# Performance work log

Hardware: AMD Instinct MI355X
Metric: run time of the kernel (lower is better)

## Reference

```python
import jax, jax.numpy as jnp
import numpy as np

NUM_ROUNDS = 3


def squash(x, axis=-1):
    # s_norm / (1 + s_norm) * x / sqrt(s_norm), matching the torch code exactly
    s_norm = jnp.sum(x * x, axis=axis, keepdims=True)
    return (s_norm / (1.0 + s_norm)) * x / jnp.sqrt(s_norm)


def setup_inputs() -> dict:
    key = jax.random.key(0)
    k1, k2 = jax.random.split(key)
    x = jax.random.normal(k1, (512, 1152, 8), dtype=jnp.float32)   # [B, R, Cin]
    W = jax.random.normal(k2, (10, 1152, 8, 16), dtype=jnp.float32)  # [N, R, Cin, Cout]
    return {"x": x, "W": W}


def reference(x, W):
    # priors = x[None,:,:,None,:] @ W[:,None,:,:,:]  -> [N, B, R, 1, Cout]
    priors = jnp.einsum('bri,nrio->nbro', x, W)[:, :, :, None, :]
    logits = jnp.zeros_like(priors)  # [N, B, R, 1, Cout]
    outps = None
    for i in range(NUM_ROUNDS):
        probs = jax.nn.softmax(logits, axis=2)  # softmax over routes R
        outps = squash(jnp.sum(probs * priors, axis=2, keepdims=True))  # [N, B, 1, 1, Cout]
        if i != NUM_ROUNDS - 1:
            # agreement logit update: dot over Cout
            logits = logits + jnp.sum(priors * outps, axis=-1, keepdims=True)
    return outps
```

## Files before the change

kernel.cpp:

```cpp
#include <hip/hip_runtime.h>
#include <math.h>

#define R_ROUTES 1152
#define CIN 8
#define COUT 16
#define BATCH 512
#define NCAPS 10
#define NUM_ROUNDS 3

typedef __fp16 h2 __attribute__((ext_vector_type(2)));
union U32H2 { unsigned int u; h2 h; };

__device__ __forceinline__ unsigned int pkrtz(float lo, float hi) {
    U32H2 v; v.h = __builtin_amdgcn_cvt_pkrtz(lo, hi);
    return v.u;
}
__device__ __forceinline__ h2 as_h2(unsigned int u) { U32H2 v; v.u = u; return v.h; }
__device__ __forceinline__ float f_lo(unsigned int u) { return (float)as_h2(u).x; }
__device__ __forceinline__ float f_hi(unsigned int u) { return (float)as_h2(u).y; }
__device__ __forceinline__ float dot2(unsigned int p, unsigned int s, float c) {
    return __builtin_amdgcn_fdot2(as_h2(p), as_h2(s), c, false);
}

#define DPP_XOR1 0xB1
#define DPP_XOR2 0x4E
#define DPP_ROR4 0x124
#define DPP_ROR8 0x128
template<int CTRL>
__device__ __forceinline__ float dpp_add(float v) {
    int d = __builtin_amdgcn_update_dpp(0, __float_as_int(v), CTRL, 0xf, 0xf, false);
    return v + __int_as_float(d);
}
__device__ __forceinline__ float p16_add(float v) {
    float a = v, b = v;
    asm("v_permlane16_swap_b32 %0, %1" : "+v"(a), "+v"(b));
    return a + b;
}
__device__ __forceinline__ float p32_add(float v) {
    float a = v, b = v;
    asm("v_permlane32_swap_b32 %0, %1" : "+v"(a), "+v"(b));
    return a + b;
}
__device__ __forceinline__ float wave_sum64(float v) {
    v = dpp_add<DPP_XOR1>(v);
    v = dpp_add<DPP_XOR2>(v);
    v = dpp_add<DPP_ROR4>(v);
    v = dpp_add<DPP_ROR8>(v);
    v = p16_add(v);
    return p32_add(v);
}

__device__ __forceinline__ int sunit(int r, int h) {
    return (2 * r + h) ^ ((r >> 2) & 7);
}

extern "C" __global__ void __launch_bounds__(256)
pack_wx(const float* __restrict__ W, const float* __restrict__ x,
        unsigned int* __restrict__ Wp, uint4* __restrict__ Xp)
{
    const int blk = blockIdx.x;
    if (blk < 720) {
        const int tau = blk * 256 + threadIdx.x;
        const int o = tau & 15;
        const int nr = tau >> 4;
        const float* __restrict__ src = W + (size_t)nr * 128 + o;
        uint4 u;
        u.x = pkrtz(src[0],  src[16]);
        u.y = pkrtz(src[32], src[48]);
        u.z = pkrtz(src[64], src[80]);
        u.w = pkrtz(src[96], src[112]);
        *(uint4*)(Wp + (size_t)tau * 4) = u;
    } else {
        const int idx = (blk - 720) * 256 + threadIdx.x;
        const float4 a = *(const float4*)(x + (size_t)idx * 8);
        const float4 b = *(const float4*)(x + (size_t)idx * 8 + 4);
        uint4 u;
        u.x = pkrtz(a.x, a.y);
        u.y = pkrtz(a.z, a.w);
        u.z = pkrtz(b.x, b.y);
        u.w = pkrtz(b.z, b.w);
        Xp[idx] = u;
    }
}

template<bool XP>
__global__ void __launch_bounds__(512, 4)
capsule_routing_v15(const float* __restrict__ x,
                    const unsigned int* __restrict__ Wp,
                    const uint4* __restrict__ Xp,
                    float* __restrict__ out)
{
    __shared__ __align__(16) unsigned int pbuf[2 * R_ROUTES * 8];
    __shared__ __align__(16) float wred[16 * 16];
    __shared__ __align__(16) float red[2 * 32 * 20];
    __shared__ float sred[2 * 4];
    __shared__ __align__(16) float sv[2 * 16];

    const int blk = blockIdx.x;
    const int n = blk >> 8;
    const int bp = blk & 255;
    const int t = threadIdx.x;

    const unsigned int* __restrict__ Wn = Wp + (size_t)n * (R_ROUTES * 64);

    float cs[2][4] = {{0.f, 0.f, 0.f, 0.f}, {0.f, 0.f, 0.f, 0.f}};
    {
        const int q = t >> 2;
        const int oq = t & 3;
        const int subw = (oq & 1) * 2;
        const int hq = oq >> 1;

        const float* __restrict__ x0 = x + (size_t)(2 * bp) * (R_ROUTES * CIN);
        const float* __restrict__ x1 = x0 + R_ROUTES * CIN;
        const uint4* __restrict__ xq0 = Xp + (size_t)(2 * bp) * R_ROUTES;
        const uint4* __restrict__ xq1 = xq0 + R_ROUTES;

        uint4 wA0, wA1, wA2, wA3, wB0, wB1, wB2, wB3;
        uint4 xA0, xA1, xB0, xB1;
        float4 gA0, gA1, gA2, gA3, gB0, gB1, gB2, gB3;

        auto loadW = [&](int it, uint4& a0, uint4& a1, uint4& a2, uint4& a3) {
            const unsigned int* wb = Wn + (size_t)(it * 128 + q) * 64 + oq * 4;
            a0 = *(const uint4*)(wb + 0);
            a1 = *(const uint4*)(wb + 16);
            a2 = *(const uint4*)(wb + 32);
            a3 = *(const uint4*)(wb + 48);
        };
        auto loadX = [&](int it, uint4& a, uint4& b,
                         float4& g0, float4& g1, float4& g2, float4& g3) {
            const int r = it * 128 + q;
            if constexpr (XP) {
                a = xq0[r];
                b = xq1[r];
            } else {
                g0 = *(const float4*)(x0 + r * 8);
                g1 = *(const float4*)(x0 + r * 8 + 4);
                g2 = *(const float4*)(x1 + r * 8);
                g3 = *(const float4*)(x1 + r * 8 + 4);
            }
        };
        auto packX = [&](uint4& a, uint4& b,
                         float4 g0, float4 g1, float4 g2, float4 g3) {
            if constexpr (!XP) {
                a.x = pkrtz(g0.x, g0.y); a.y = pkrtz(g0.z, g0.w);
                a.z = pkrtz(g1.x, g1.y); a.w = pkrtz(g1.z, g1.w);
                b.x = pkrtz(g2.x, g2.y); b.y = pkrtz(g2.z, g2.w);
                b.z = pkrtz(g3.x, g3.y); b.w = pkrtz(g3.z, g3.w);
            }
        };
        auto compute = [&](int it, uint4 w0, uint4 w1, uint4 w2, uint4 w3,
                           uint4 xa, uint4 xb) {
            const int r = it * 128 + q;
            {
                const float p0 = dot2(w0.w, xa.w, dot2(w0.z, xa.z, dot2(w0.y, xa.y, dot2(w0.x, xa.x, 0.f))));
                const float p1 = dot2(w1.w, xa.w, dot2(w1.z, xa.z, dot2(w1.y, xa.y, dot2(w1.x, xa.x, 0.f))));
                const float p2 = dot2(w2.w, xa.w, dot2(w2.z, xa.z, dot2(w2.y, xa.y, dot2(w2.x, xa.x, 0.f))));
                const float p3 = dot2(w3.w, xa.w, dot2(w3.z, xa.z, dot2(w3.y, xa.y, dot2(w3.x, xa.x, 0.f))));
                cs[0][0] += p0; cs[0][1] += p1; cs[0][2] += p2; cs[0][3] += p3;
                uint2 u; u.x = pkrtz(p0, p1); u.y = pkrtz(p2, p3);
                *(uint2*)(pbuf + sunit(r, hq) * 4 + subw) = u;
            }
            {
                const float p0 = dot2(w0.w, xb.w, dot2(w0.z, xb.z, dot2(w0.y, xb.y, dot2(w0.x, xb.x, 0.f))));
                const float p1 = dot2(w1.w, xb.w, dot2(w1.z, xb.z, dot2(w1.y, xb.y, dot2(w1.x, xb.x, 0.f))));
                const float p2 = dot2(w2.w, xb.w, dot2(w2.z, xb.z, dot2(w2.y, xb.y, dot2(w2.x, xb.x, 0.f))));
                const float p3 = dot2(w3.w, xb.w, dot2(w3.z, xb.z, dot2(w3.y, xb.y, dot2(w3.x, xb.x, 0.f))));
                cs[1][0] += p0; cs[1][1] += p1; cs[1][2] += p2; cs[1][3] += p3;
                uint2 u; u.x = pkrtz(p0, p1); u.y = pkrtz(p2, p3);
                *(uint2*)(pbuf + R_ROUTES * 8 + sunit(r, hq) * 4 + subw) = u;
            }
        };

        loadW(0, wA0, wA1, wA2, wA3);
        loadX(0, xA0, xA1, gA0, gA1, gA2, gA3);
        #pragma unroll 1
        for (int it = 0; it < 8; it += 2) {
            loadW(it + 1, wB0, wB1, wB2, wB3);
            loadX(it + 1, xB0, xB1, gB0, gB1, gB2, gB3);
            packX(xA0, xA1, gA0, gA1, gA2, gA3);
            compute(it, wA0, wA1, wA2, wA3, xA0, xA1);
            loadW(it + 2, wA0, wA1, wA2, wA3);
            loadX(it + 2, xA0, xA1, gA0, gA1, gA2, gA3);
            packX(xB0, xB1, gB0, gB1, gB2, gB3);
            compute(it + 1, wB0, wB1, wB2, wB3, xB0, xB1);
        }
        packX(xA0, xA1, gA0, gA1, gA2, gA3);
        compute(8, wA0, wA1, wA2, wA3, xA0, xA1);

        #pragma unroll
        for (int b = 0; b < 2; ++b)
            #pragma unroll
            for (int j = 0; j < 4; ++j) {
                float v = cs[b][j];
                v = dpp_add<DPP_ROR4>(v);
                v = dpp_add<DPP_ROR8>(v);
                v = p16_add(v);
                v = p32_add(v);
                cs[b][j] = v;
            }
        if ((t & 63) < 4) {
            const int w = t >> 6;
            *(float4*)(wred + (w * 2 + 0) * 16 + 4 * oq) =
                make_float4(cs[0][0], cs[0][1], cs[0][2], cs[0][3]);
            *(float4*)(wred + (w * 2 + 1) * 16 + 4 * oq) =
                make_float4(cs[1][0], cs[1][1], cs[1][2], cs[1][3]);
        }
    }
    __syncthreads();

    const int half = t >> 8;
    const int tt = t & 255;
    unsigned int* __restrict__ pb = pbuf + half * (R_ROUTES * 8);
    float* __restrict__ redh = red + half * (32 * 20);
    float* __restrict__ sredh = sred + half * 4;
    float* __restrict__ svh = sv + half * 16;

    if (tt < 64) {
        const int k = tt & 15, wg = tt >> 4;
        float s = wred[(wg * 2 + half) * 16 + k] + wred[((wg + 4) * 2 + half) * 16 + k];
        s = p16_add(s);
        s = p32_add(s);
        if (tt < 16) svh[tt] = s * (1.0f / (float)R_ROUTES);
    }
    __syncthreads();

    float4 s0 = *(const float4*)(svh + 0);
    float4 s1 = *(const float4*)(svh + 4);
    float4 s2 = *(const float4*)(svh + 8);
    float4 s3 = *(const float4*)(svh + 12);
    float sn = s0.x * s0.x;
    sn = fmaf(s0.y, s0.y, sn); sn = fmaf(s0.z, s0.z, sn); sn = fmaf(s0.w, s0.w, sn);
    sn = fmaf(s1.x, s1.x, sn); sn = fmaf(s1.y, s1.y, sn); sn = fmaf(s1.z, s1.z, sn);
    sn = fmaf(s1.w, s1.w, sn);
    sn = fmaf(s2.x, s2.x, sn); sn = fmaf(s2.y, s2.y, sn); sn = fmaf(s2.z, s2.z, sn);
    sn = fmaf(s2.w, s2.w, sn);
    sn = fmaf(s3.x, s3.x, sn); sn = fmaf(s3.y, s3.y, sn); sn = fmaf(s3.z, s3.z, sn);
    sn = fmaf(s3.w, s3.w, sn);
    float factor = sn / ((1.0f + sn) * sqrtf(sn));

    const int nr = (tt < 128) ? 5 : 4;
    float bl[5] = {0.f, 0.f, 0.f, 0.f, 0.f};

    #pragma unroll 1
    for (int pass = 1; pass < NUM_ROUNDS; ++pass) {
        unsigned int svp[8];
        svp[0] = pkrtz(s0.x, s0.y); svp[1] = pkrtz(s0.z, s0.w);
        svp[2] = pkrtz(s1.x, s1.y); svp[3] = pkrtz(s1.z, s1.w);
        svp[4] = pkrtz(s2.x, s2.y); svp[5] = pkrtz(s2.z, s2.w);
        svp[6] = pkrtz(s3.x, s3.y); svp[7] = pkrtz(s3.z, s3.w);
        float acc[16];
        #pragma unroll
        for (int o = 0; o < 16; ++o) acc[o] = 0.f;
        float es = 0.f;

        #pragma unroll
        for (int k = 0; k < 5; ++k) {
            if (k < nr) {
                const int r = tt + (k << 8);
                const uint4 a = *(const uint4*)(pb + sunit(r, 0) * 4);
                const uint4 c = *(const uint4*)(pb + sunit(r, 1) * 4);
                float d = 0.f;
                d = dot2(a.x, svp[0], d);
                d = dot2(a.y, svp[1], d);
                d = dot2(a.z, svp[2], d);
                d = dot2(a.w, svp[3], d);
                d = dot2(c.x, svp[4], d);
                d = dot2(c.y, svp[5], d);
                d = dot2(c.z, svp[6], d);
                d = dot2(c.w, svp[7], d);
                bl[k] = fmaf(factor, d, bl[k]);
                const float e = __expf(bl[k]);
                es += e;
                acc[0]  = fmaf(e, f_lo(a.x), acc[0]);
                acc[1]  = fmaf(e, f_hi(a.x), acc[1]);
                acc[2]  = fmaf(e, f_lo(a.y), acc[2]);
                acc[3]  = fmaf(e, f_hi(a.y), acc[3]);
                acc[4]  = fmaf(e, f_lo(a.z), acc[4]);
                acc[5]  = fmaf(e, f_hi(a.z), acc[5]);
                acc[6]  = fmaf(e, f_lo(a.w), acc[6]);
                acc[7]  = fmaf(e, f_hi(a.w), acc[7]);
                acc[8]  = fmaf(e, f_lo(c.x), acc[8]);
                acc[9]  = fmaf(e, f_hi(c.x), acc[9]);
                acc[10] = fmaf(e, f_lo(c.y), acc[10]);
                acc[11] = fmaf(e, f_hi(c.y), acc[11]);
                acc[12] = fmaf(e, f_lo(c.z), acc[12]);
                acc[13] = fmaf(e, f_hi(c.z), acc[13]);
                acc[14] = fmaf(e, f_lo(c.w), acc[14]);
                acc[15] = fmaf(e, f_hi(c.w), acc[15]);
            }
        }
        es = wave_sum64(es);
        if ((t & 63) == 0) sredh[tt >> 6] = es;

        #pragma unroll
        for (int o = 0; o < 16; ++o) {
            float v = acc[o];
            v = dpp_add<DPP_XOR1>(v);
            v = dpp_add<DPP_XOR2>(v);
            v = dpp_add<DPP_ROR4>(v);
            acc[o] = v;
        }
        if ((tt & 7) == 0) {
            float* dst = redh + (tt >> 3) * 20;
            *(float4*)(dst + 0)  = make_float4(acc[0],  acc[1],  acc[2],  acc[3]);
            *(float4*)(dst + 4)  = make_float4(acc[4],  acc[5],  acc[6],  acc[7]);
            *(float4*)(dst + 8)  = make_float4(acc[8],  acc[9],  acc[10], acc[11]);
            *(float4*)(dst + 12) = make_float4(acc[12], acc[13], acc[14], acc[15]);
        }
        __syncthreads();

        if (tt < 64) {
            const int k = tt & 15, wg = tt >> 4;
            float s = 0.f;
            #pragma unroll
            for (int i = 0; i < 8; ++i) s += redh[(wg * 8 + i) * 20 + k];
            s = p16_add(s);
            s = p32_add(s);
            if (tt < 16) {
                const float Z = sredh[0] + sredh[1] + sredh[2] + sredh[3];
                svh[tt] = s / Z;
            }
        }
        __syncthreads();

        s0 = *(const float4*)(svh + 0);
        s1 = *(const float4*)(svh + 4);
        s2 = *(const float4*)(svh + 8);
        s3 = *(const float4*)(svh + 12);
        sn = s0.x * s0.x;
        sn = fmaf(s0.y, s0.y, sn); sn = fmaf(s0.z, s0.z, sn); sn = fmaf(s0.w, s0.w, sn);
        sn = fmaf(s1.x, s1.x, sn); sn = fmaf(s1.y, s1.y, sn); sn = fmaf(s1.z, s1.z, sn);
        sn = fmaf(s1.w, s1.w, sn);
        sn = fmaf(s2.x, s2.x, sn); sn = fmaf(s2.y, s2.y, sn); sn = fmaf(s2.z, s2.z, sn);
        sn = fmaf(s2.w, s2.w, sn);
        sn = fmaf(s3.x, s3.x, sn); sn = fmaf(s3.y, s3.y, sn); sn = fmaf(s3.z, s3.z, sn);
        sn = fmaf(s3.w, s3.w, sn);
        factor = sn / ((1.0f + sn) * sqrtf(sn));
    }

    if (tt < 16) {
        const int o = (tt >> 2) + ((tt & 3) << 2);
        out[((size_t)n * BATCH + 2 * bp + half) * COUT + o] = factor * svh[tt];
    }
}

extern "C" void kernel_launch(void* const* d_in, const int* in_sizes, int n_in,
                              void* d_out, int out_size, void* d_ws, size_t ws_size,
                              hipStream_t stream) {
    const float* x = (const float*)d_in[0];
    const float* W = (const float*)d_in[1];
    float* out = (float*)d_out;

    unsigned int* Wp = (unsigned int*)d_ws;
    const size_t WPB = (size_t)NCAPS * R_ROUTES * COUT * 16;
    const size_t XPB = (size_t)BATCH * R_ROUTES * 16;
    uint4* Xp = (uint4*)((char*)d_ws + WPB);

    if (ws_size >= WPB + XPB) {
        pack_wx<<<dim3(720 + 2304), dim3(256), 0, stream>>>(W, x, Wp, Xp);
        capsule_routing_v15<true><<<dim3(NCAPS * (BATCH / 2)), dim3(512), 0, stream>>>(x, Wp, Xp, out);
    } else {
        pack_wx<<<dim3(720), dim3(256), 0, stream>>>(W, x, Wp, Xp);
        capsule_routing_v15<false><<<dim3(NCAPS * (BATCH / 2)), dim3(512), 0, stream>>>(x, Wp, Xp, out);
    }
}
```

Before: 128.3 us.

## Assign one batch element per block and split routes across both halves

After: 146.3 us. 1.14x slower.

```diff
diff --git a/kernel.cpp b/kernel.cpp
--- a/kernel.cpp
+++ b/kernel.cpp
@@ -32,13 +32,19 @@
     return v + __int_as_float(d);
 }
 __device__ __forceinline__ float p16_add(float v) {
-    float a = v, b = v;
-    asm("v_permlane16_swap_b32 %0, %1" : "+v"(a), "+v"(b));
+    float a, b;
+    asm("v_mov_b32 %0, %2\n\t"
+        "v_mov_b32 %1, %2\n\t"
+        "v_permlane16_swap_b32 %0, %1"
+        : "=&v"(a), "=&v"(b) : "v"(v));
     return a + b;
 }
 __device__ __forceinline__ float p32_add(float v) {
-    float a = v, b = v;
-    asm("v_permlane32_swap_b32 %0, %1" : "+v"(a), "+v"(b));
+    float a, b;
+    asm("v_mov_b32 %0, %2\n\t"
+        "v_mov_b32 %1, %2\n\t"
+        "v_permlane32_swap_b32 %0, %1"
+        : "=&v"(a), "=&v"(b) : "v"(v));
     return a + b;
 }
 __device__ __forceinline__ float wave_sum64(float v) {
@@ -85,149 +91,116 @@
 
 template<bool XP>
 __global__ void __launch_bounds__(512, 4)
-capsule_routing_v15(const float* __restrict__ x,
+capsule_routing_v16(const float* __restrict__ x,
                     const unsigned int* __restrict__ Wp,
                     const uint4* __restrict__ Xp,
                     float* __restrict__ out)
 {
-    __shared__ __align__(16) unsigned int pbuf[2 * R_ROUTES * 8];
-    __shared__ __align__(16) float wred[16 * 16];
+    __shared__ __align__(16) unsigned int pbuf[R_ROUTES * 8];
+    __shared__ __align__(16) float wred[8 * 16];
     __shared__ __align__(16) float red[2 * 32 * 20];
-    __shared__ float sred[2 * 4];
-    __shared__ __align__(16) float sv[2 * 16];
+    __shared__ __align__(16) float sred[2 * 4];
+    __shared__ __align__(16) float sv[16];
 
     const int blk = blockIdx.x;
-    const int n = blk >> 8;
-    const int bp = blk & 255;
+    const int n = blk >> 9;
+    const int b = blk & 511;
     const int t = threadIdx.x;
 
     const unsigned int* __restrict__ Wn = Wp + (size_t)n * (R_ROUTES * 64);
 
-    float cs[2][4] = {{0.f, 0.f, 0.f, 0.f}, {0.f, 0.f, 0.f, 0.f}};
+    float cs[4] = {0.f, 0.f, 0.f, 0.f};
     {
         const int q = t >> 2;
         const int oq = t & 3;
         const int subw = (oq & 1) * 2;
         const int hq = oq >> 1;
 
-        const float* __restrict__ x0 = x + (size_t)(2 * bp) * (R_ROUTES * CIN);
-        const float* __restrict__ x1 = x0 + R_ROUTES * CIN;
-        const uint4* __restrict__ xq0 = Xp + (size_t)(2 * bp) * R_ROUTES;
-        const uint4* __restrict__ xq1 = xq0 + R_ROUTES;
+        const float* __restrict__ x0 = x + (size_t)b * (R_ROUTES * CIN);
+        const uint4* __restrict__ xq0 = Xp + (size_t)b * R_ROUTES;
 
         uint4 wA0, wA1, wA2, wA3, wB0, wB1, wB2, wB3;
-        uint4 xA0, xA1, xB0, xB1;
-        float4 gA0, gA1, gA2, gA3, gB0, gB1, gB2, gB3;
+        uint4 xA, xB;
 
         auto loadW = [&](int it, uint4& a0, uint4& a1, uint4& a2, uint4& a3) {
-            const unsigned int* wb = Wn + (size_t)(it * 128 + q) * 64 + oq * 4;
-            a0 = *(const uint4*)(wb + 0);
-            a1 = *(const uint4*)(wb + 16);
-            a2 = *(const uint4*)(wb + 32);
-            a3 = *(const uint4*)(wb + 48);
+            const unsigned int* wb = Wn + (size_t)(it * 128 + q) * 64;
+            a0 = *(const uint4*)(wb + (oq + 0) * 4);
+            a1 = *(const uint4*)(wb + (oq + 4) * 4);
+            a2 = *(const uint4*)(wb + (oq + 8) * 4);
+            a3 = *(const uint4*)(wb + (oq + 12) * 4);
         };
-        auto loadX = [&](int it, uint4& a, uint4& b,
-                         float4& g0, float4& g1, float4& g2, float4& g3) {
+        auto loadX = [&](int it, uint4& xa) {
             const int r = it * 128 + q;
             if constexpr (XP) {
-                a = xq0[r];
-                b = xq1[r];
+                xa = xq0[r];
             } else {
-                g0 = *(const float4*)(x0 + r * 8);
-                g1 = *(const float4*)(x0 + r * 8 + 4);
-                g2 = *(const float4*)(x1 + r * 8);
-                g3 = *(const float4*)(x1 + r * 8 + 4);
+                const float4 g0 = *(const float4*)(x0 + r * 8);
+                const float4 g1 = *(const float4*)(x0 + r * 8 + 4);
+                xa.x = pkrtz(g0.x, g0.y); xa.y = pkrtz(g0.z, g0.w);
+                xa.z = pkrtz(g1.x, g1.y); xa.w = pkrtz(g1.z, g1.w);
             }
         };
-        auto packX = [&](uint4& a, uint4& b,
-                         float4 g0, float4 g1, float4 g2, float4 g3) {
-            if constexpr (!XP) {
-                a.x = pkrtz(g0.x, g0.y); a.y = pkrtz(g0.z, g0.w);
-                a.z = pkrtz(g1.x, g1.y); a.w = pkrtz(g1.z, g1.w);
-                b.x = pkrtz(g2.x, g2.y); b.y = pkrtz(g2.z, g2.w);
-                b.z = pkrtz(g3.x, g3.y); b.w = pkrtz(g3.z, g3.w);
-            }
+        auto compute = [&](int it, const uint4& w0, const uint4& w1,
+                           const uint4& w2, const uint4& w3, const uint4& xa) {
+            const int r = it * 128 + q;
+            const float p0 = dot2(w0.w, xa.w, dot2(w0.z, xa.z, dot2(w0.y, xa.y, dot2(w0.x, xa.x, 0.f))));
+            const float p1 = dot2(w1.w, xa.w, dot2(w1.z, xa.z, dot2(w1.y, xa.y, dot2(w1.x, xa.x, 0.f))));
+            const float p2 = dot2(w2.w, xa.w, dot2(w2.z, xa.z, dot2(w2.y, xa.y, dot2(w2.x, xa.x, 0.f))));
+            const float p3 = dot2(w3.w, xa.w, dot2(w3.z, xa.z, dot2(w3.y, xa.y, dot2(w3.x, xa.x, 0.f))));
+            cs[0] += p0; cs[1] += p1; cs[2] += p2; cs[3] += p3;
+            uint2 u; u.x = pkrtz(p0, p1); u.y = pkrtz(p2, p3);
+            *(uint2*)(pbuf + sunit(r, hq) * 4 + subw) = u;
         };
-        auto compute = [&](int it, uint4 w0, uint4 w1, uint4 w2, uint4 w3,
-                           uint4 xa, uint4 xb) {
-            const int r = it * 128 + q;
-            {
-                const float p0 = dot2(w0.w, xa.w, dot2(w0.z, xa.z, dot2(w0.y, xa.y, dot2(w0.x, xa.x, 0.f))));
-                const float p1 = dot2(w1.w, xa.w, dot2(w1.z, xa.z, dot2(w1.y, xa.y, dot2(w1.x, xa.x, 0.f))));
-                const float p2 = dot2(w2.w, xa.w, dot2(w2.z, xa.z, dot2(w2.y, xa.y, dot2(w2.x, xa.x, 0.f))));
-                const float p3 = dot2(w3.w, xa.w, dot2(w3.z, xa.z, dot2(w3.y, xa.y, dot2(w3.x, xa.x, 0.f))));
-                cs[0][0] += p0; cs[0][1] += p1; cs[0][2] += p2; cs[0][3] += p3;
-                uint2 u; u.x = pkrtz(p0, p1); u.y = pkrtz(p2, p3);
-                *(uint2*)(pbuf + sunit(r, hq) * 4 + subw) = u;
-            }
-            {
-                const float p0 = dot2(w0.w, xb.w, dot2(w0.z, xb.z, dot2(w0.y, xb.y, dot2(w0.x, xb.x, 0.f))));
-                const float p1 = dot2(w1.w, xb.w, dot2(w1.z, xb.z, dot2(w1.y, xb.y, dot2(w1.x, xb.x, 0.f))));
-                const float p2 = dot2(w2.w, xb.w, dot2(w2.z, xb.z, dot2(w2.y, xb.y, dot2(w2.x, xb.x, 0.f))));
-                const float p3 = dot2(w3.w, xb.w, dot2(w3.z, xb.z, dot2(w3.y, xb.y, dot2(w3.x, xb.x, 0.f))));
-                cs[1][0] += p0; cs[1][1] += p1; cs[1][2] += p2; cs[1][3] += p3;
-                uint2 u; u.x = pkrtz(p0, p1); u.y = pkrtz(p2, p3);
-                *(uint2*)(pbuf + R_ROUTES * 8 + sunit(r, hq) * 4 + subw) = u;
-            }
-        };
 
         loadW(0, wA0, wA1, wA2, wA3);
-        loadX(0, xA0, xA1, gA0, gA1, gA2, gA3);
+        loadX(0, xA);
         #pragma unroll 1
         for (int it = 0; it < 8; it += 2) {
             loadW(it + 1, wB0, wB1, wB2, wB3);
-            loadX(it + 1, xB0, xB1, gB0, gB1, gB2, gB3);
-            packX(xA0, xA1, gA0, gA1, gA2, gA3);
-            compute(it, wA0, wA1, wA2, wA3, xA0, xA1);
+            loadX(it + 1, xB);
+            compute(it, wA0, wA1, wA2, wA3, xA);
             loadW(it + 2, wA0, wA1, wA2, wA3);
-            loadX(it + 2, xA0, xA1, gA0, gA1, gA2, gA3);
-            packX(xB0, xB1, gB0, gB1, gB2, gB3);
-            compute(it + 1, wB0, wB1, wB2, wB3, xB0, xB1);
-        }
-        packX(xA0, xA1, gA0, gA1, gA2, gA3);
-        compute(8, wA0, wA1, wA2, wA3, xA0, xA1);
+            loadX(it + 2, xA);
+            compute(it + 1, wB0, wB1, wB2, wB3, xB);
+        }
+        compute(8, wA0, wA1, wA2, wA3, xA);
 
         #pragma unroll
-        for (int b = 0; b < 2; ++b)
-            #pragma unroll
-            for (int j = 0; j < 4; ++j) {
-                float v = cs[b][j];
-                v = dpp_add<DPP_ROR4>(v);
-                v = dpp_add<DPP_ROR8>(v);
-                v = p16_add(v);
-                v = p32_add(v);
-                cs[b][j] = v;
-            }
+        for (int j = 0; j < 4; ++j) {
+            float v = cs[j];
+            v = dpp_add<DPP_ROR4>(v);
+            v = dpp_add<DPP_ROR8>(v);
+            v = p16_add(v);
+            v = p32_add(v);
+            cs[j] = v;
+        }
         if ((t & 63) < 4) {
             const int w = t >> 6;
-            *(float4*)(wred + (w * 2 + 0) * 16 + 4 * oq) =
-                make_float4(cs[0][0], cs[0][1], cs[0][2], cs[0][3]);
-            *(float4*)(wred + (w * 2 + 1) * 16 + 4 * oq) =
-                make_float4(cs[1][0], cs[1][1], cs[1][2], cs[1][3]);
-        }
+            *(float4*)(wred + w * 16 + 4 * oq) =
+                make_float4(cs[0], cs[1], cs[2], cs[3]);
+        }
+    }
+    __syncthreads();
+
+    if (t < 64) {
+        const int k = t & 15, wg = t >> 4;
+        float s = wred[wg * 16 + k] + wred[(wg + 4) * 16 + k];
+        s = p16_add(s);
+        s = p32_add(s);
+        if (t < 16) sv[t] = s * (1.0f / (float)R_ROUTES);
     }
     __syncthreads();
 
     const int half = t >> 8;
     const int tt = t & 255;
-    unsigned int* __restrict__ pb = pbuf + half * (R_ROUTES * 8);
     float* __restrict__ redh = red + half * (32 * 20);
     float* __restrict__ sredh = sred + half * 4;
-    float* __restrict__ svh = sv + half * 16;
-
-    if (tt < 64) {
-        const int k = tt & 15, wg = tt >> 4;
-        float s = wred[(wg * 2 + half) * 16 + k] + wred[((wg + 4) * 2 + half) * 16 + k];
-        s = p16_add(s);
-        s = p32_add(s);
-        if (tt < 16) svh[tt] = s * (1.0f / (float)R_ROUTES);
-    }
-    __syncthreads();
-
-    float4 s0 = *(const float4*)(svh + 0);
-    float4 s1 = *(const float4*)(svh + 4);
-    float4 s2 = *(const float4*)(svh + 8);
-    float4 s3 = *(const float4*)(svh + 12);
+    const int rbase = half * 576;
+
+    float4 s0 = *(const float4*)(sv + 0);
+    float4 s1 = *(const float4*)(sv + 4);
+    float4 s2 = *(const float4*)(sv + 8);
+    float4 s3 = *(const float4*)(sv + 12);
     float sn = s0.x * s0.x;
     sn = fmaf(s0.y, s0.y, sn); sn = fmaf(s0.z, s0.z, sn); sn = fmaf(s0.w, s0.w, sn);
     sn = fmaf(s1.x, s1.x, sn); sn = fmaf(s1.y, s1.y, sn); sn = fmaf(s1.z, s1.z, sn);
@@ -238,8 +211,8 @@
     sn = fmaf(s3.w, s3.w, sn);
     float factor = sn / ((1.0f + sn) * sqrtf(sn));
 
-    const int nr = (tt < 128) ? 5 : 4;
-    float bl[5] = {0.f, 0.f, 0.f, 0.f, 0.f};
+    const int nr = (tt < 64) ? 3 : 2;
+    float bl[3] = {0.f, 0.f, 0.f};
 
     #pragma unroll 1
     for (int pass = 1; pass < NUM_ROUNDS; ++pass) {
@@ -248,17 +221,18 @@
         svp[2] = pkrtz(s1.x, s1.y); svp[3] = pkrtz(s1.z, s1.w);
         svp[4] = pkrtz(s2.x, s2.y); svp[5] = pkrtz(s2.z, s2.w);
         svp[6] = pkrtz(s3.x, s3.y); svp[7] = pkrtz(s3.z, s3.w);
+
         float acc[16];
         #pragma unroll
         for (int o = 0; o < 16; ++o) acc[o] = 0.f;
         float es = 0.f;
 
         #pragma unroll
-        for (int k = 0; k < 5; ++k) {
+        for (int k = 0; k < 3; ++k) {
             if (k < nr) {
-                const int r = tt + (k << 8);
-                const uint4 a = *(const uint4*)(pb + sunit(r, 0) * 4);
-                const uint4 c = *(const uint4*)(pb + sunit(r, 1) * 4);
+                const int r = rbase + tt + (k << 8);
+                const uint4 a = *(const uint4*)(pbuf + sunit(r, 0) * 4);
+                const uint4 c = *(const uint4*)(pbuf + sunit(r, 1) * 4);
                 float d = 0.f;
                 d = dot2(a.x, svp[0], d);
                 d = dot2(a.y, svp[1], d);
@@ -289,6 +263,7 @@
                 acc[15] = fmaf(e, f_hi(c.w), acc[15]);
             }
         }
+
         es = wave_sum64(es);
         if ((t & 63) == 0) sredh[tt >> 6] = es;
 
@@ -309,24 +284,26 @@
         }
         __syncthreads();
 
-        if (tt < 64) {
-            const int k = tt & 15, wg = tt >> 4;
+        if (t < 64) {
+            const int k = t & 15, wg = t >> 4;
             float s = 0.f;
             #pragma unroll
-            for (int i = 0; i < 8; ++i) s += redh[(wg * 8 + i) * 20 + k];
+            for (int i = 0; i < 8; ++i)
+                s += red[(wg * 8 + i) * 20 + k] + red[(32 + wg * 8 + i) * 20 + k];
             s = p16_add(s);
             s = p32_add(s);
-            if (tt < 16) {
-                const float Z = sredh[0] + sredh[1] + sredh[2] + sredh[3];
-                svh[tt] = s / Z;
-            }
+            const float4 z0 = *(const float4*)(sred);
+            const float4 z1 = *(const float4*)(sred + 4);
+            const float Z = ((z0.x + z0.y) + (z0.z + z0.w)) +
+                            ((z1.x + z1.y) + (z1.z + z1.w));
+            if (t < 16) sv[t] = s / Z;
         }
         __syncthreads();
 
-        s0 = *(const float4*)(svh + 0);
-        s1 = *(const float4*)(svh + 4);
-        s2 = *(const float4*)(svh + 8);
-        s3 = *(const float4*)(svh + 12);
+        s0 = *(const float4*)(sv + 0);
+        s1 = *(const float4*)(sv + 4);
+        s2 = *(const float4*)(sv + 8);
+        s3 = *(const float4*)(sv + 12);
         sn = s0.x * s0.x;
         sn = fmaf(s0.y, s0.y, sn); sn = fmaf(s0.z, s0.z, sn); sn = fmaf(s0.w, s0.w, sn);
         sn = fmaf(s1.x, s1.x, sn); sn = fmaf(s1.y, s1.y, sn); sn = fmaf(s1.z, s1.z, sn);
@@ -338,9 +315,9 @@
         factor = sn / ((1.0f + sn) * sqrtf(sn));
     }
 
-    if (tt < 16) {
-        const int o = (tt >> 2) + ((tt & 3) << 2);
-        out[((size_t)n * BATCH + 2 * bp + half) * COUT + o] = factor * svh[tt];
+    if (t < 16) {
+        const int o = (t >> 2) + ((t & 3) << 2);
+        out[((size_t)n * BATCH + b) * COUT + o] = factor * sv[t];
     }
 }
 
@@ -358,9 +335,9 @@
 
     if (ws_size >= WPB + XPB) {
         pack_wx<<<dim3(720 + 2304), dim3(256), 0, stream>>>(W, x, Wp, Xp);
-        capsule_routing_v15<true><<<dim3(NCAPS * (BATCH / 2)), dim3(512), 0, stream>>>(x, Wp, Xp, out);
+        capsule_routing_v16<true><<<dim3(NCAPS * BATCH), dim3(512), 0, stream>>>(x, Wp, Xp, out);
     } else {
         pack_wx<<<dim3(720), dim3(256), 0, stream>>>(W, x, Wp, Xp);
-        capsule_routing_v15<false><<<dim3(NCAPS * (BATCH / 2)), dim3(512), 0, stream>>>(x, Wp, Xp, out);
-    }
-}
+        capsule_routing_v16<false><<<dim3(NCAPS * BATCH), dim3(512), 0, stream>>>(x, Wp, Xp, out);
+    }
+}
```

## Double block size to 1024 threads, halving per-thread priors and routing work

Applied to the files above, without the earlier changes.

After: 151.3 us. 1.18x slower.

```diff
diff --git a/kernel.cpp b/kernel.cpp
--- a/kernel.cpp
+++ b/kernel.cpp
@@ -32,13 +32,19 @@
     return v + __int_as_float(d);
 }
 __device__ __forceinline__ float p16_add(float v) {
-    float a = v, b = v;
-    asm("v_permlane16_swap_b32 %0, %1" : "+v"(a), "+v"(b));
+    float a, b;
+    asm("v_mov_b32 %0, %2\n\t"
+        "v_mov_b32 %1, %2\n\t"
+        "v_permlane16_swap_b32 %0, %1"
+        : "=&v"(a), "=&v"(b) : "v"(v));
     return a + b;
 }
 __device__ __forceinline__ float p32_add(float v) {
-    float a = v, b = v;
-    asm("v_permlane32_swap_b32 %0, %1" : "+v"(a), "+v"(b));
+    float a, b;
+    asm("v_mov_b32 %0, %2\n\t"
+        "v_mov_b32 %1, %2\n\t"
+        "v_permlane32_swap_b32 %0, %1"
+        : "=&v"(a), "=&v"(b) : "v"(v));
     return a + b;
 }
 __device__ __forceinline__ float wave_sum64(float v) {
@@ -48,6 +54,13 @@
     v = dpp_add<DPP_ROR8>(v);
     v = p16_add(v);
     return p32_add(v);
+}
+__device__ __forceinline__ float sum16_rows(float v) {
+    v = dpp_add<DPP_XOR1>(v);
+    v = dpp_add<DPP_XOR2>(v);
+    v = dpp_add<DPP_ROR4>(v);
+    v = dpp_add<DPP_ROR8>(v);
+    return v;
 }
 
 __device__ __forceinline__ int sunit(int r, int h) {
@@ -84,16 +97,16 @@
 }
 
 template<bool XP>
-__global__ void __launch_bounds__(512, 4)
-capsule_routing_v15(const float* __restrict__ x,
+__global__ void __launch_bounds__(1024, 4)
+capsule_routing_v17(const float* __restrict__ x,
                     const unsigned int* __restrict__ Wp,
                     const uint4* __restrict__ Xp,
                     float* __restrict__ out)
 {
     __shared__ __align__(16) unsigned int pbuf[2 * R_ROUTES * 8];
-    __shared__ __align__(16) float wred[16 * 16];
+    __shared__ __align__(16) float wred[32 * 16];
     __shared__ __align__(16) float red[2 * 32 * 20];
-    __shared__ float sred[2 * 4];
+    __shared__ __align__(16) float sred[2 * 8];
     __shared__ __align__(16) float sv[2 * 16];
 
     const int blk = blockIdx.x;
@@ -103,121 +116,102 @@
 
     const unsigned int* __restrict__ Wn = Wp + (size_t)n * (R_ROUTES * 64);
 
-    float cs[2][4] = {{0.f, 0.f, 0.f, 0.f}, {0.f, 0.f, 0.f, 0.f}};
+    float cs[2][2] = {{0.f, 0.f}, {0.f, 0.f}};
     {
-        const int q = t >> 2;
-        const int oq = t & 3;
-        const int subw = (oq & 1) * 2;
-        const int hq = oq >> 1;
+        const int q = t >> 3;
+        const int oq = t & 7;
 
         const float* __restrict__ x0 = x + (size_t)(2 * bp) * (R_ROUTES * CIN);
         const float* __restrict__ x1 = x0 + R_ROUTES * CIN;
         const uint4* __restrict__ xq0 = Xp + (size_t)(2 * bp) * R_ROUTES;
         const uint4* __restrict__ xq1 = xq0 + R_ROUTES;
-
-        uint4 wA0, wA1, wA2, wA3, wB0, wB1, wB2, wB3;
+        const unsigned int* __restrict__ wbase = Wn + (size_t)q * 64 + oq * 4;
+
+        uint4 wA0, wA1, wB0, wB1;
         uint4 xA0, xA1, xB0, xB1;
-        float4 gA0, gA1, gA2, gA3, gB0, gB1, gB2, gB3;
-
-        auto loadW = [&](int it, uint4& a0, uint4& a1, uint4& a2, uint4& a3) {
-            const unsigned int* wb = Wn + (size_t)(it * 128 + q) * 64 + oq * 4;
+
+        auto loadW = [&](int it, uint4& a0, uint4& a1) {
+            const unsigned int* wb = wbase + (size_t)it * (128 * 64);
             a0 = *(const uint4*)(wb + 0);
-            a1 = *(const uint4*)(wb + 16);
-            a2 = *(const uint4*)(wb + 32);
-            a3 = *(const uint4*)(wb + 48);
+            a1 = *(const uint4*)(wb + 32);
         };
-        auto loadX = [&](int it, uint4& a, uint4& b,
-                         float4& g0, float4& g1, float4& g2, float4& g3) {
+        auto loadX = [&](int it, uint4& xa, uint4& xb) {
             const int r = it * 128 + q;
             if constexpr (XP) {
-                a = xq0[r];
-                b = xq1[r];
+                xa = xq0[r];
+                xb = xq1[r];
             } else {
-                g0 = *(const float4*)(x0 + r * 8);
-                g1 = *(const float4*)(x0 + r * 8 + 4);
-                g2 = *(const float4*)(x1 + r * 8);
-                g3 = *(const float4*)(x1 + r * 8 + 4);
+                const float4 g0 = *(const float4*)(x0 + r * 8);
+                const float4 g1 = *(const float4*)(x0 + r * 8 + 4);
+                const float4 g2 = *(const float4*)(x1 + r * 8);
+                const float4 g3 = *(const float4*)(x1 + r * 8 + 4);
+                xa.x = pkrtz(g0.x, g0.y); xa.y = pkrtz(g0.z, g0.w);
+                xa.z = pkrtz(g1.x, g1.y); xa.w = pkrtz(g1.z, g1.w);
+                xb.x = pkrtz(g2.x, g2.y); xb.y = pkrtz(g2.z, g2.w);
+                xb.z = pkrtz(g3.x, g3.y); xb.w = pkrtz(g3.z, g3.w);
             }
         };
-        auto packX = [&](uint4& a, uint4& b,
-                         float4 g0, float4 g1, float4 g2, float4 g3) {
-            if constexpr (!XP) {
-                a.x = pkrtz(g0.x, g0.y); a.y = pkrtz(g0.z, g0.w);
-                a.z = pkrtz(g1.x, g1.y); a.w = pkrtz(g1.z, g1.w);
-                b.x = pkrtz(g2.x, g2.y); b.y = pkrtz(g2.z, g2.w);
-                b.z = pkrtz(g3.x, g3.y); b.w = pkrtz(g3.z, g3.w);
+        auto compute = [&](int it, const uint4& w0, const uint4& w1,
+                           const uint4& xa, const uint4& xb) {
+            const int r = it * 128 + q;
+            const int ui = sunit(r, oq >> 2) * 4 + (oq & 3);
+            {
+                const float pa = dot2(w0.w, xa.w, dot2(w0.z, xa.z, dot2(w0.y, xa.y, dot2(w0.x, xa.x, 0.f))));
+                const float pb = dot2(w1.w, xa.w, dot2(w1.z, xa.z, dot2(w1.y, xa.y, dot2(w1.x, xa.x, 0.f))));
+                cs[0][0] += pa; cs[0][1] += pb;
+                pbuf[ui] = pkrtz(pa, pb);
+            }
+            {
+                const float pa = dot2(w0.w, xb.w, dot2(w0.z, xb.z, dot2(w0.y, xb.y, dot2(w0.x, xb.x, 0.f))));
+                const float pb = dot2(w1.w, xb.w, dot2(w1.z, xb.z, dot2(w1.y, xb.y, dot2(w1.x, xb.x, 0.f))));
+                cs[1][0] += pa; cs[1][1] += pb;
+                pbuf[R_ROUTES * 8 + ui] = pkrtz(pa, pb);
             }
         };
-        auto compute = [&](int it, uint4 w0, uint4 w1, uint4 w2, uint4 w3,
-                           uint4 xa, uint4 xb) {
-            const int r = it * 128 + q;
-            {
-                const float p0 = dot2(w0.w, xa.w, dot2(w0.z, xa.z, dot2(w0.y, xa.y, dot2(w0.x, xa.x, 0.f))));
-                const float p1 = dot2(w1.w, xa.w, dot2(w1.z, xa.z, dot2(w1.y, xa.y, dot2(w1.x, xa.x, 0.f))));
-                const float p2 = dot2(w2.w, xa.w, dot2(w2.z, xa.z, dot2(w2.y, xa.y, dot2(w2.x, xa.x, 0.f))));
-                const float p3 = dot2(w3.w, xa.w, dot2(w3.z, xa.z, dot2(w3.y, xa.y, dot2(w3.x, xa.x, 0.f))));
-                cs[0][0] += p0; cs[0][1] += p1; cs[0][2] += p2; cs[0][3] += p3;
-                uint2 u; u.x = pkrtz(p0, p1); u.y = pkrtz(p2, p3);
-                *(uint2*)(pbuf + sunit(r, hq) * 4 + subw) = u;
-            }
-            {
-                const float p0 = dot2(w0.w, xb.w, dot2(w0.z, xb.z, dot2(w0.y, xb.y, dot2(w0.x, xb.x, 0.f))));
-                const float p1 = dot2(w1.w, xb.w, dot2(w1.z, xb.z, dot2(w1.y, xb.y, dot2(w1.x, xb.x, 0.f))));
-                const float p2 = dot2(w2.w, xb.w, dot2(w2.z, xb.z, dot2(w2.y, xb.y, dot2(w2.x, xb.x, 0.f))));
-                const float p3 = dot2(w3.w, xb.w, dot2(w3.z, xb.z, dot2(w3.y, xb.y, dot2(w3.x, xb.x, 0.f))));
-                cs[1][0] += p0; cs[1][1] += p1; cs[1][2] += p2; cs[1][3] += p3;
-                uint2 u; u.x = pkrtz(p0, p1); u.y = pkrtz(p2, p3);
-                *(uint2*)(pbuf + R_ROUTES * 8 + sunit(r, hq) * 4 + subw) = u;
-            }
-        };
-
-        loadW(0, wA0, wA1, wA2, wA3);
-        loadX(0, xA0, xA1, gA0, gA1, gA2, gA3);
+
+        loadW(0, wA0, wA1);
+        loadX(0, xA0, xA1);
         #pragma unroll 1
         for (int it = 0; it < 8; it += 2) {
-            loadW(it + 1, wB0, wB1, wB2, wB3);
-            loadX(it + 1, xB0, xB1, gB0, gB1, gB2, gB3);
-            packX(xA0, xA1, gA0, gA1, gA2, gA3);
-            compute(it, wA0, wA1, wA2, wA3, xA0, xA1);
-            loadW(it + 2, wA0, wA1, wA2, wA3);
-            loadX(it + 2, xA0, xA1, gA0, gA1, gA2, gA3);
-            packX(xB0, xB1, gB0, gB1, gB2, gB3);
-            compute(it + 1, wB0, wB1, wB2, wB3, xB0, xB1);
-        }
-        packX(xA0, xA1, gA0, gA1, gA2, gA3);
-        compute(8, wA0, wA1, wA2, wA3, xA0, xA1);
+            loadW(it + 1, wB0, wB1);
+            loadX(it + 1, xB0, xB1);
+            compute(it, wA0, wA1, xA0, xA1);
+            loadW(it + 2, wA0, wA1);
+            loadX(it + 2, xA0, xA1);
+            compute(it + 1, wB0, wB1, xB0, xB1);
+        }
+        compute(8, wA0, wA1, xA0, xA1);
 
         #pragma unroll
         for (int b = 0; b < 2; ++b)
             #pragma unroll
-            for (int j = 0; j < 4; ++j) {
+            for (int j = 0; j < 2; ++j) {
                 float v = cs[b][j];
-                v = dpp_add<DPP_ROR4>(v);
                 v = dpp_add<DPP_ROR8>(v);
                 v = p16_add(v);
                 v = p32_add(v);
                 cs[b][j] = v;
             }
-        if ((t & 63) < 4) {
+        if ((t & 63) < 8) {
             const int w = t >> 6;
-            *(float4*)(wred + (w * 2 + 0) * 16 + 4 * oq) =
-                make_float4(cs[0][0], cs[0][1], cs[0][2], cs[0][3]);
-            *(float4*)(wred + (w * 2 + 1) * 16 + 4 * oq) =
-                make_float4(cs[1][0], cs[1][1], cs[1][2], cs[1][3]);
+            *(float2*)(wred + (w * 2 + 0) * 16 + 2 * oq) = make_float2(cs[0][0], cs[0][1]);
+            *(float2*)(wred + (w * 2 + 1) * 16 + 2 * oq) = make_float2(cs[1][0], cs[1][1]);
         }
     }
     __syncthreads();
 
-    const int half = t >> 8;
-    const int tt = t & 255;
+    const int half = t >> 9;
+    const int tt = t & 511;
     unsigned int* __restrict__ pb = pbuf + half * (R_ROUTES * 8);
     float* __restrict__ redh = red + half * (32 * 20);
-    float* __restrict__ sredh = sred + half * 4;
+    float* __restrict__ sredh = sred + half * 8;
     float* __restrict__ svh = sv + half * 16;
 
     if (tt < 64) {
         const int k = tt & 15, wg = tt >> 4;
-        float s = wred[(wg * 2 + half) * 16 + k] + wred[((wg + 4) * 2 + half) * 16 + k];
+        float s = 0.f;
+        #pragma unroll
+        for (int i = 0; i < 4; ++i) s += wred[((wg * 4 + i) * 2 + half) * 16 + k];
         s = p16_add(s);
         s = p32_add(s);
         if (tt < 16) svh[tt] = s * (1.0f / (float)R_ROUTES);
@@ -238,8 +232,8 @@
     sn = fmaf(s3.w, s3.w, sn);
     float factor = sn / ((1.0f + sn) * sqrtf(sn));
 
-    const int nr = (tt < 128) ? 5 : 4;
-    float bl[5] = {0.f, 0.f, 0.f, 0.f, 0.f};
+    const int nr = (tt < 128) ? 3 : 2;
+    float bl[3] = {0.f, 0.f, 0.f};
 
     #pragma unroll 1
     for (int pass = 1; pass < NUM_ROUNDS; ++pass) {
@@ -248,15 +242,16 @@
         svp[2] = pkrtz(s1.x, s1.y); svp[3] = pkrtz(s1.z, s1.w);
         svp[4] = pkrtz(s2.x, s2.y); svp[5] = pkrtz(s2.z, s2.w);
         svp[6] = pkrtz(s3.x, s3.y); svp[7] = pkrtz(s3.z, s3.w);
+
         float acc[16];
         #pragma unroll
         for (int o = 0; o < 16; ++o) acc[o] = 0.f;
         float es = 0.f;
 
         #pragma unroll
-        for (int k = 0; k < 5; ++k) {
+        for (int k = 0; k < 3; ++k) {
             if (k < nr) {
-                const int r = tt + (k << 8);
+                const int r = tt + (k << 9);
                 const uint4 a = *(const uint4*)(pb + sunit(r, 0) * 4);
                 const uint4 c = *(const uint4*)(pb + sunit(r, 1) * 4);
                 float d = 0.f;
@@ -289,19 +284,14 @@
                 acc[15] = fmaf(e, f_hi(c.w), acc[15]);
             }
         }
+
         es = wave_sum64(es);
         if ((t & 63) == 0) sredh[tt >> 6] = es;
 
         #pragma unroll
-        for (int o = 0; o < 16; ++o) {
-            float v = acc[o];
-            v = dpp_add<DPP_XOR1>(v);
-            v = dpp_add<DPP_XOR2>(v);
-            v = dpp_add<DPP_ROR4>(v);
-            acc[o] = v;
-        }
-        if ((tt & 7) == 0) {
-            float* dst = redh + (tt >> 3) * 20;
+        for (int o = 0; o < 16; ++o) acc[o] = sum16_rows(acc[o]);
+        if ((tt & 15) == 0) {
+            float* dst = redh + (tt >> 4) * 20;
             *(float4*)(dst + 0)  = make_float4(acc[0],  acc[1],  acc[2],  acc[3]);
             *(float4*)(dst + 4)  = make_float4(acc[4],  acc[5],  acc[6],  acc[7]);
             *(float4*)(dst + 8)  = make_float4(acc[8],  acc[9],  acc[10], acc[11]);
@@ -317,7 +307,10 @@
             s = p16_add(s);
             s = p32_add(s);
             if (tt < 16) {
-                const float Z = sredh[0] + sredh[1] + sredh[2] + sredh[3];
+                const float4 z0 = *(const float4*)(sredh);
+                const float4 z1 = *(const float4*)(sredh + 4);
+                const float Z = ((z0.x + z0.y) + (z0.z + z0.w)) +
+                                ((z1.x + z1.y) + (z1.z + z1.w));
                 svh[tt] = s / Z;
             }
         }
@@ -339,7 +332,7 @@
     }
 
     if (tt < 16) {
-        const int o = (tt >> 2) + ((tt & 3) << 2);
+        const int o = (tt >> 1) + ((tt & 1) << 3);
         out[((size_t)n * BATCH + 2 * bp + half) * COUT + o] = factor * svh[tt];
     }
 }
@@ -358,9 +351,9 @@
 
     if (ws_size >= WPB + XPB) {
         pack_wx<<<dim3(720 + 2304), dim3(256), 0, stream>>>(W, x, Wp, Xp);
-        capsule_routing_v15<true><<<dim3(NCAPS * (BATCH / 2)), dim3(512), 0, stream>>>(x, Wp, Xp, out);
+        capsule_routing_v17<true><<<dim3(NCAPS * (BATCH / 2)), dim3(1024), 0, stream>>>(x, Wp, Xp, out);
     } else {
         pack_wx<<<dim3(720), dim3(256), 0, stream>>>(W, x, Wp, Xp);
-        capsule_routing_v15<false><<<dim3(NCAPS * (BATCH / 2)), dim3(512), 0, stream>>>(x, Wp, Xp, out);
-    }
-}
+        capsule_routing_v17<false><<<dim3(NCAPS * (BATCH / 2)), dim3(1024), 0, stream>>>(x, Wp, Xp, out);
+    }
+}
```
